# Optimization experiments

Hardware: AMD Instinct MI355X
Metric: run time of the kernel (lower is better)

Reference implementation:

```python
import jax, jax.numpy as jnp
import numpy as np

N = 50000      # nodes
E = 800000     # edges (before self-loops)
DIN = 384
D = 128        # hidden_dim == output_dim
H = 4          # heads
FH = D // H    # per-head dim
B = 64         # graphs in batch
NEG = 0.2      # LeakyReLU slope in GATConv
EPS = 1e-5     # LayerNorm eps


def setup_inputs() -> dict:
    key = jax.random.key(0)
    ks = jax.random.split(key, 24)
    s = 0.02
    inp = {
        'node_features': jax.random.normal(ks[0], (N, DIN), jnp.float32),
        'edge_index': jax.random.randint(ks[1], (2, E), 0, N, dtype=jnp.int64),
        'edge_weight': jax.random.uniform(ks[2], (E,), jnp.float32),
        'batch': jnp.sort(jax.random.randint(ks[3], (N,), 0, B, dtype=jnp.int64)),
        # input projection
        'Wp': jax.random.normal(ks[4], (DIN, D), jnp.float32) * s,
        'bp': jnp.zeros((D,), jnp.float32),
    }
    for l in range(2):
        o = 5 + l * 9
        inp[f'W{l}'] = jax.random.normal(ks[o], (D, D), jnp.float32) * s      # lin_src (shared src/dst)
        inp[f'as{l}'] = jax.random.normal(ks[o + 1], (H, FH), jnp.float32) * s  # att_src
        inp[f'ad{l}'] = jax.random.normal(ks[o + 2], (H, FH), jnp.float32) * s  # att_dst
        inp[f'We{l}'] = jax.random.normal(ks[o + 3], (D,), jnp.float32) * s   # lin_edge (edge_dim=1)
        inp[f'ae{l}'] = jax.random.normal(ks[o + 4], (H, FH), jnp.float32) * s  # att_edge
        inp[f'b{l}'] = jnp.zeros((D,), jnp.float32)                           # GATConv bias
        inp[f'g{l}'] = jnp.ones((D,), jnp.float32)                            # LayerNorm gamma
        inp[f'be{l}'] = jnp.zeros((D,), jnp.float32)                          # LayerNorm beta
    return inp


def _gat(x, src, dst, ew, W, a_s, a_d, We, a_e, b):
    """PyG GATConv(in, D/H, heads=H, edge_dim=1), eval mode. ew includes self-loops."""
    n = x.shape[0]
    h = (x @ W).reshape(n, H, FH)                      # [N,H,FH]
    a_src = jnp.einsum('nhf,hf->nh', h, a_s)           # [N,H]
    a_dst = jnp.einsum('nhf,hf->nh', h, a_d)
    e = (ew[:, None] * We[None, :]).reshape(-1, H, FH)  # edge_dim=1 linear, no bias
    a_eg = jnp.einsum('ehf,hf->eh', e, a_e)            # [E,H]
    alpha = jax.nn.leaky_relu(a_src[src] + a_dst[dst] + a_eg, NEG)
    # softmax over incoming edges of each dst node
    amax = jax.ops.segment_max(alpha, dst, num_segments=n)
    amax = jnp.where(jnp.isfinite(amax), amax, 0.0)
    ex = jnp.exp(alpha - amax[dst])
    denom = jax.ops.segment_sum(ex, dst, num_segments=n)
    coef = ex / (denom[dst] + 1e-16)                   # [E,H]
    msg = h[src] * coef[..., None]                     # [E,H,FH]
    out = jax.ops.segment_sum(msg, dst, num_segments=n).reshape(n, D)
    return out + b


def _ln(x, g, b):
    mu = x.mean(-1, keepdims=True)
    v = ((x - mu) ** 2).mean(-1, keepdims=True)
    return (x - mu) * jax.lax.rsqrt(v + EPS) * g + b


def reference(node_features, edge_index, edge_weight, batch, Wp, bp,
              W0, as0, ad0, We0, ae0, b0, g0, be0,
              W1, as1, ad1, We1, ae1, b1, g1, be1):
    n = node_features.shape[0]
    # PyG GATConv add_self_loops=True, fill_value='mean' for edge_attr
    loop = jnp.arange(n, dtype=edge_index.dtype)
    src = jnp.concatenate([edge_index[0], loop])
    dst = jnp.concatenate([edge_index[1], loop])
    ew = jnp.concatenate([edge_weight, jnp.full((n,), edge_weight.mean(), edge_weight.dtype)])

    x = node_features @ Wp + bp
    for (W, a_s, a_d, We, a_e, b, g, be) in (
        (W0, as0, ad0, We0, ae0, b0, g0, be0),
        (W1, as1, ad1, We1, ae1, b1, g1, be1),
    ):
        res = x
        y = _gat(x, src, dst, ew, W, a_s, a_d, We, a_e, b)
        y = jax.nn.elu(_ln(y, g, be))
        x = y + res  # shapes match (hidden == output)

    # global_mean_pool
    s = jax.ops.segment_sum(x, batch, num_segments=B)
    c = jax.ops.segment_sum(jnp.ones((n,), x.dtype), batch, num_segments=B)
    return s / jnp.maximum(c, 1.0)[:, None]
```

## Files before the change

kernel.cpp:

```cpp
#include <hip/hip_runtime.h>

#define N_NODES 50000
#define N_EDGES 800000
#define DIN 384
#define DH 128
#define NB 64
#define NEG 0.2f

__device__ __forceinline__ float bf2f(unsigned short u) {
    return __uint_as_float((unsigned)u << 16);
}
__device__ __forceinline__ unsigned short f2bf(float x) {
    unsigned u = __float_as_uint(x);
    return (unsigned short)((u + 0x7fff + ((u >> 16) & 1)) >> 16);
}
__device__ __forceinline__ float sel4(float4 v, int k) {
    float r = v.x;
    r = (k == 1) ? v.y : r;
    r = (k == 2) ? v.z : r;
    r = (k == 3) ? v.w : r;
    return r;
}
using us8 = __attribute__((ext_vector_type(8))) unsigned short;
using short8 = __attribute__((ext_vector_type(8))) short;
using f32x4  = __attribute__((ext_vector_type(4))) float;

__global__ __launch_bounds__(256) void histew_kernel(const int* __restrict__ dst,
        const float* __restrict__ ew, int* __restrict__ cnt,
        int* __restrict__ rank, float* __restrict__ ews,
        const float* __restrict__ Wp, const float* __restrict__ W0,
        const float* __restrict__ W1,
        const float* __restrict__ as0, const float* __restrict__ ad0,
        const float* __restrict__ as1, const float* __restrict__ ad1,
        unsigned short* __restrict__ Wtp, unsigned short* __restrict__ Wt0,
        unsigned short* __restrict__ Wt1) {
    __shared__ float sred[4];
    const int tid = threadIdx.x;
    const int pi = blockIdx.x * 256 + tid;
    if (blockIdx.x < 192) {
        const int k = pi >> 7, n = pi & 127;
        Wtp[(size_t)n * DIN + k] = f2bf(Wp[pi]);
        if (pi < DH * DH) {
            Wt0[(size_t)n * DH + k] = f2bf(W0[pi]);
            Wt1[(size_t)n * DH + k] = f2bf(W1[pi]);
        }
    } else if (blockIdx.x < 196) {
        const int b = blockIdx.x - 192;
        const int layer = b >> 1, sd = b & 1;
        const float* Ws = layer ? W1 : W0;
        const float* av = layer ? (sd ? ad1 : as1) : (sd ? ad0 : as0);
        unsigned short* Wt = layer ? Wt1 : Wt0;
        #pragma unroll
        for (int rep = 0; rep < 2; ++rep) {
            const int idx = rep * 256 + tid;
            const int k = idx >> 2, hd = idx & 3;
            float s = 0.f;
            for (int f = 0; f < 32; ++f)
                s += Ws[k * DH + hd * 32 + f] * av[hd * 32 + f];
            Wt[(size_t)(128 + sd * 4 + hd) * DH + k] = f2bf(s);
        }
    }
    float v = 0.0f;
    for (int i = blockIdx.x * 256 + tid; i < N_EDGES; i += gridDim.x * 256) {
        rank[i] = atomicAdd(&cnt[dst[i]], 1);
        v += ew[i];
    }
    #pragma unroll
    for (int o = 32; o; o >>= 1) v += __shfl_down(v, o, 64);
    if ((tid & 63) == 0) sred[tid >> 6] = v;
    __syncthreads();
    if (tid == 0) atomicAdd(ews, sred[0] + sred[1] + sred[2] + sred[3]);
}

#define SB 196
__global__ __launch_bounds__(256) void scan_a(const int* __restrict__ cnt,
                       int* __restrict__ scanned, int* __restrict__ bsums,
                       const float* __restrict__ We0, const float* __restrict__ ae0,
                       const float* __restrict__ We1, const float* __restrict__ ae1,
                       const float* __restrict__ ews, float* __restrict__ consts) {
    __shared__ int s[256];
    const int tid = threadIdx.x;
    if (blockIdx.x < SB) {
        int i = blockIdx.x * 256 + tid;
        int v = (i < N_NODES) ? cnt[i] : 0;
        s[tid] = v; __syncthreads();
        for (int o = 1; o < 256; o <<= 1) {
            int t = (tid >= o) ? s[tid - o] : 0;
            __syncthreads();
            s[tid] += t;
            __syncthreads();
        }
        if (i < N_NODES) scanned[i] = s[tid] - v;
        if (tid == 255) bsums[blockIdx.x] = s[255];
    } else if (tid < 64) {
        const int l = tid;
        float p00 = We0[l] * ae0[l];
        float p01 = We0[l + 64] * ae0[l + 64];
        float p10 = We1[l] * ae1[l];
        float p11 = We1[l + 64] * ae1[l + 64];
        #pragma unroll
        for (int o = 1; o < 32; o <<= 1) {
            p00 += __shfl_xor(p00, o, 64); p01 += __shfl_xor(p01, o, 64);
            p10 += __shfl_xor(p10, o, 64); p11 += __shfl_xor(p11, o, 64);
        }
        const float c0 = __shfl(p00, 0, 64), c1 = __shfl(p00, 32, 64);
        const float c2 = __shfl(p01, 0, 64), c3 = __shfl(p01, 32, 64);
        const float d0 = __shfl(p10, 0, 64), d1 = __shfl(p10, 32, 64);
        const float d2 = __shfl(p11, 0, 64), d3 = __shfl(p11, 32, 64);
        if (l == 0) {
            consts[0] = c0; consts[1] = c1; consts[2] = c2; consts[3] = c3;
            consts[4] = d0; consts[5] = d1; consts[6] = d2; consts[7] = d3;
            consts[8] = ews[0] * (1.0f / N_EDGES);
        }
    }
}

__global__ __launch_bounds__(256) void scan_bc(const int* __restrict__ scanned,
                        const int* __restrict__ bsums,
                        const int* __restrict__ cnt, int* __restrict__ ptr) {
    __shared__ int red[4];
    const int tid = threadIdx.x;
    int part = 0;
    for (int j = tid; j < blockIdx.x; j += 256) part += bsums[j];
    #pragma unroll
    for (int o = 32; o; o >>= 1) part += __shfl_down(part, o, 64);
    if ((tid & 63) == 0) red[tid >> 6] = part;
    __syncthreads();
    const int off = red[0] + red[1] + red[2] + red[3];
    const int i = blockIdx.x * 256 + tid;
    if (i < N_NODES) {
        const int p = scanned[i] + off;
        ptr[i] = p;
        if (i == N_NODES - 1) ptr[N_NODES] = p + cnt[i];
    }
}

#define PROJB 782
__global__ __launch_bounds__(256) void fillproj_kernel(
    const int* __restrict__ src, const int* __restrict__ dst,
    const float* __restrict__ ew, const int* __restrict__ rank,
    const int* __restrict__ ptr, int2* __restrict__ recE,
    const float* __restrict__ A, const unsigned short* __restrict__ Wt,
    const float* __restrict__ bias, float* __restrict__ C,
    unsigned short* __restrict__ Cb, int M)
{
    constexpr int K = DIN, BM = 64, BK = 32, LS = 40;
    __shared__ unsigned short As[BM * LS];
    __shared__ unsigned short Bs[DH * LS];
    const int tid = threadIdx.x;

    if (blockIdx.x >= PROJB) {
        const int e0 = ((blockIdx.x - PROJB) * 256 + tid) * 4;
        if (e0 >= N_EDGES) return;
        const int4 d4 = *(const int4*)(dst + e0);
        const int4 s4 = *(const int4*)(src + e0);
        const int4 r4 = *(const int4*)(rank + e0);
        const float4 w4 = *(const float4*)(ew + e0);
        recE[ptr[d4.x] + r4.x] = make_int2(s4.x, __float_as_int(w4.x));
        recE[ptr[d4.y] + r4.y] = make_int2(s4.y, __float_as_int(w4.y));
        recE[ptr[d4.z] + r4.z] = make_int2(s4.z, __float_as_int(w4.z));
        recE[ptr[d4.w] + r4.w] = make_int2(s4.w, __float_as_int(w4.w));
        return;
    }

    const int w = tid >> 6, l = tid & 63;
    const int lane16 = l & 15, quad = l >> 4;
    const int m0 = blockIdx.x * BM;

    f32x4 acc[8] = {};

    const int ar = tid >> 2, a4 = tid & 3;
    int arow = m0 + ar; if (arow >= M) arow = M - 1;
    const float* Ap = A + (size_t)arow * K;

    for (int k0 = 0; k0 < K; k0 += BK) {
        __syncthreads();
        #pragma unroll
        for (int i = 0; i < 2; ++i) {
            const int f4 = a4 + 4 * i;
            float4 v = *(const float4*)(Ap + k0 + f4 * 4);
            ushort4 u = {f2bf(v.x), f2bf(v.y), f2bf(v.z), f2bf(v.w)};
            *(ushort4*)&As[ar * LS + f4 * 4] = u;
        }
        #pragma unroll
        for (int i = 0; i < 2; ++i) {
            const int idx = tid + 256 * i;
            const int bn = idx >> 2, seg = idx & 3;
            us8 v = *(const us8*)(Wt + (size_t)bn * K + k0 + seg * 8);
            *(us8*)&Bs[bn * LS + seg * 8] = v;
        }
        __syncthreads();
        short8 afr = *(short8*)&As[(w * 16 + lane16) * LS + quad * 8];
        #pragma unroll
        for (int nt = 0; nt < 8; ++nt) {
            short8 bf = *(short8*)&Bs[(nt * 16 + lane16) * LS + quad * 8];
            acc[nt] = __builtin_amdgcn_mfma_f32_16x16x32_bf16(afr, bf, acc[nt], 0, 0, 0);
        }
    }

    const int orow0 = m0 + w * 16 + quad * 4;
    #pragma unroll
    for (int nt = 0; nt < 8; ++nt) {
        const int col = nt * 16 + lane16;
        const float bv = bias[col];
        #pragma unroll
        for (int r = 0; r < 4; ++r) {
            const int row = orow0 + r;
            if (row < M) {
                const float v = acc[nt][r] + bv;
                C[(size_t)row * DH + col] = v;
                Cb[(size_t)row * DH + col] = f2bf(v);
            }
        }
    }
}

__global__ __launch_bounds__(256) void mfma_gemm_layer(
    const unsigned short* __restrict__ Ab, const unsigned short* __restrict__ Wt,
    unsigned short* __restrict__ Hout, int M,
    float* __restrict__ asrc_o, float* __restrict__ adst_o)
{
    constexpr int K = DH, BM = 64, BK = 32, LS = 40;
    __shared__ unsigned short As[BM * LS];
    __shared__ unsigned short Bs[144 * LS];

    const int tid = threadIdx.x;
    const int w = tid >> 6, l = tid & 63;
    const int lane16 = l & 15, quad = l >> 4;
    const int m0 = blockIdx.x * BM;

    f32x4 acc[9] = {};

    const int ar = tid >> 2, aseg = tid & 3;
    int arow = m0 + ar; if (arow >= M) arow = M - 1;
    const unsigned short* Ap = Ab + (size_t)arow * K;

    for (int k0 = 0; k0 < K; k0 += BK) {
        __syncthreads();
        {
            us8 v = *(const us8*)(Ap + k0 + aseg * 8);
            *(us8*)&As[ar * LS + aseg * 8] = v;
        }
        #pragma unroll
        for (int i = 0; i < 3; ++i) {
            const int idx = tid + 256 * i;
            if (idx < 576) {
                const int bn = idx >> 2, seg = idx & 3;
                us8 v = *(const us8*)(Wt + (size_t)bn * K + k0 + seg * 8);
                *(us8*)&Bs[bn * LS + seg * 8] = v;
            }
        }
        __syncthreads();
        short8 af = *(short8*)&As[(w * 16 + lane16) * LS + quad * 8];
        #pragma unroll
        for (int nt = 0; nt < 9; ++nt) {
            short8 bf = *(short8*)&Bs[(nt * 16 + lane16) * LS + quad * 8];
            acc[nt] = __builtin_amdgcn_mfma_f32_16x16x32_bf16(af, bf, acc[nt], 0, 0, 0);
        }
    }

    const int orow0 = m0 + w * 16 + quad * 4;
    #pragma unroll
    for (int nt = 0; nt < 8; ++nt) {
        const int col = nt * 16 + lane16;
        #pragma unroll
        for (int r = 0; r < 4; ++r) {
            const int row = orow0 + r;
            if (row < M)
                Hout[(size_t)row * DH + col] = f2bf(acc[nt][r]);
        }
    }
    #pragma unroll
    for (int r = 0; r < 4; ++r) {
        const int row = orow0 + r;
        if (row < M && lane16 < 8) {
            if (lane16 < 4) asrc_o[(size_t)row * 4 + lane16] = acc[8][r];
            else            adst_o[(size_t)row * 4 + (lane16 - 4)] = acc[8][r];
        }
    }
}

__device__ __forceinline__ void msg_node(
    const int n, const int c8, const int hd8,
    const float cc_l, const float ewm,
    const unsigned short* __restrict__ h,
    const float* __restrict__ asrc, const float* __restrict__ adst,
    const float* __restrict__ xres,
    const int* __restrict__ indptr, const int2* __restrict__ recE,
    const float* __restrict__ bias, const float* __restrict__ gamma,
    const float* __restrict__ beta, float z[8])
{
    const unsigned short* hb = h + c8 * 8;
    const int st = indptr[n];
    const int deg = indptr[n + 1] - st;
    const float ad_l = adst[(size_t)n * 4 + hd8];
    const float as_l = asrc[(size_t)n * 4 + hd8];

    float a0 = as_l + ad_l + ewm * cc_l;
    a0 = a0 > 0.f ? a0 : NEG * a0;
    const float pv0_l = __expf(a0);

    float dsum = 0.f;
    float acc8[8];
    {
        us8 u = *(const us8*)(hb + (size_t)n * DH);
        #pragma unroll
        for (int i = 0; i < 8; ++i) acc8[i] = pv0_l * bf2f(u[i]);
    }

    const int2* rq = recE + st;
    int e = 0;
    for (; e + 3 < deg; e += 4) {
        const int2 r0 = rq[e],     r1 = rq[e + 1];
        const int2 r2 = rq[e + 2], r3 = rq[e + 3];
        const float av0 = asrc[(size_t)r0.x * 4 + hd8];
        const float av1 = asrc[(size_t)r1.x * 4 + hd8];
        const float av2 = asrc[(size_t)r2.x * 4 + hd8];
        const float av3 = asrc[(size_t)r3.x * 4 + hd8];
        us8 u0 = *(const us8*)(hb + (size_t)r0.x * DH);
        us8 u1 = *(const us8*)(hb + (size_t)r1.x * DH);
        us8 u2 = *(const us8*)(hb + (size_t)r2.x * DH);
        us8 u3 = *(const us8*)(hb + (size_t)r3.x * DH);
        float al0 = av0 + ad_l + __int_as_float(r0.y) * cc_l;
        float al1 = av1 + ad_l + __int_as_float(r1.y) * cc_l;
        float al2 = av2 + ad_l + __int_as_float(r2.y) * cc_l;
        float al3 = av3 + ad_l + __int_as_float(r3.y) * cc_l;
        al0 = al0 > 0.f ? al0 : NEG * al0;
        al1 = al1 > 0.f ? al1 : NEG * al1;
        al2 = al2 > 0.f ? al2 : NEG * al2;
        al3 = al3 > 0.f ? al3 : NEG * al3;
        const float c0 = __expf(al0), c1 = __expf(al1);
        const float c2 = __expf(al2), c3 = __expf(al3);
        dsum += (c0 + c1) + (c2 + c3);
        #pragma unroll
        for (int i = 0; i < 8; ++i)
            acc8[i] = fmaf(c0, bf2f(u0[i]),
                      fmaf(c1, bf2f(u1[i]),
                      fmaf(c2, bf2f(u2[i]),
                      fmaf(c3, bf2f(u3[i]), acc8[i]))));
    }
    for (; e < deg; ++e) {
        const int2 r = rq[e];
        const float av = asrc[(size_t)r.x * 4 + hd8];
        us8 u = *(const us8*)(hb + (size_t)r.x * DH);
        float al = av + ad_l + __int_as_float(r.y) * cc_l;
        al = al > 0.f ? al : NEG * al;
        const float c = __expf(al);
        dsum += c;
        #pragma unroll
        for (int i = 0; i < 8; ++i) acc8[i] = fmaf(c, bf2f(u[i]), acc8[i]);
    }

    const float inv_d = 1.0f / (dsum + pv0_l + 1e-16f);
    const float4 b4a = *(const float4*)(bias + c8 * 8);
    const float4 b4b = *(const float4*)(bias + c8 * 8 + 4);
    float y[8];
    y[0] = acc8[0] * inv_d + b4a.x; y[1] = acc8[1] * inv_d + b4a.y;
    y[2] = acc8[2] * inv_d + b4a.z; y[3] = acc8[3] * inv_d + b4a.w;
    y[4] = acc8[4] * inv_d + b4b.x; y[5] = acc8[5] * inv_d + b4b.y;
    y[6] = acc8[6] * inv_d + b4b.z; y[7] = acc8[7] * inv_d + b4b.w;

    float s1 = 0.f, s2 = 0.f;
    #pragma unroll
    for (int i = 0; i < 8; ++i) { s1 += y[i]; s2 += y[i] * y[i]; }
    #pragma unroll
    for (int o = 1; o < 16; o <<= 1) {
        s1 += __shfl_xor(s1, o, 64);
        s2 += __shfl_xor(s2, o, 64);
    }
    const float mu = s1 * (1.0f / DH);
    const float var = s2 * (1.0f / DH) - mu * mu;
    const float rs = rsqrtf(var + 1e-5f);

    const float4 g4a = *(const float4*)(gamma + c8 * 8);
    const float4 g4b = *(const float4*)(gamma + c8 * 8 + 4);
    const float4 e4a = *(const float4*)(beta + c8 * 8);
    const float4 e4b = *(const float4*)(beta + c8 * 8 + 4);
    const float4 r4a = *(const float4*)(xres + (size_t)n * DH + c8 * 8);
    const float4 r4b = *(const float4*)(xres + (size_t)n * DH + c8 * 8 + 4);
    const float gv[8] = {g4a.x, g4a.y, g4a.z, g4a.w, g4b.x, g4b.y, g4b.z, g4b.w};
    const float ev[8] = {e4a.x, e4a.y, e4a.z, e4a.w, e4b.x, e4b.y, e4b.z, e4b.w};
    const float rv[8] = {r4a.x, r4a.y, r4a.z, r4a.w, r4b.x, r4b.y, r4b.z, r4b.w};
    #pragma unroll
    for (int i = 0; i < 8; ++i) {
        float t = (y[i] - mu) * rs * gv[i] + ev[i];
        z[i] = (t > 0.f ? t : __expf(t) - 1.0f) + rv[i];
    }
}

#define MSG_NPB 16
__global__ __launch_bounds__(256) void msg_main_kernel(
    const unsigned short* __restrict__ h, const float* __restrict__ asrc,
    const float* __restrict__ adst, const float* __restrict__ xres,
    const int* __restrict__ indptr, const int2* __restrict__ recE,
    const float* __restrict__ consts, const int layer,
    const float* __restrict__ bias, const float* __restrict__ gamma,
    const float* __restrict__ beta, float* __restrict__ xout,
    unsigned short* __restrict__ xob)
{
    const int l = threadIdx.x & 63;
    const int wv = threadIdx.x >> 6;
    const int grp = l >> 4, c8 = l & 15, hd8 = c8 >> 2;
    const int n = blockIdx.x * MSG_NPB + wv * 4 + grp;

    const float cc_l = sel4(*(const float4*)(consts + layer * 4), hd8);
    const float ewm = consts[8];

    float z[8];
    msg_node(n, c8, hd8, cc_l, ewm, h, asrc, adst, xres, indptr, recE,
             bias, gamma, beta, z);

    *(float4*)(xout + (size_t)n * DH + c8 * 8)     = *(float4*)&z[0];
    *(float4*)(xout + (size_t)n * DH + c8 * 8 + 4) = *(float4*)&z[4];
    if (xob) {
        ushort4 ub0 = {f2bf(z[0]), f2bf(z[1]), f2bf(z[2]), f2bf(z[3])};
        ushort4 ub1 = {f2bf(z[4]), f2bf(z[5]), f2bf(z[6]), f2bf(z[7])};
        *(ushort4*)(xob + (size_t)n * DH + c8 * 8)     = ub0;
        *(ushort4*)(xob + (size_t)n * DH + c8 * 8 + 4) = ub1;
    }
}

#define PNODES 64
__global__ __launch_bounds__(128) void pool_kernel(const float* __restrict__ x,
        const int* __restrict__ batch, float* __restrict__ pool, int* __restrict__ gcnt)
{
    int t = threadIdx.x;
    int n0 = blockIdx.x * PNODES;
    if (n0 >= N_NODES) return;
    int n1 = min(n0 + PNODES, N_NODES);
    float acc = 0.f; int cn = 0;
    int curb = batch[n0];
    for (int n = n0; n < n1; ++n) {
        int b = batch[n];
        if (b != curb) {
            atomicAdd(&pool[(size_t)curb * DH + t], acc);
            if (t == 0) atomicAdd(&gcnt[curb], cn);
            acc = 0.f; cn = 0; curb = b;
        }
        acc += x[(size_t)n * DH + t];
        ++cn;
    }
    atomicAdd(&pool[(size_t)curb * DH + t], acc);
    if (t == 0) atomicAdd(&gcnt[curb], cn);
}

__global__ void div_kernel(const float* __restrict__ pool, const int* __restrict__ gcnt,
                           float* __restrict__ out)
{
    int i = blockIdx.x * blockDim.x + threadIdx.x;
    if (i < NB * DH) {
        float c = (float)gcnt[i >> 7];
        out[i] = pool[i] / fmaxf(c, 1.0f);
    }
}

extern "C" void kernel_launch(void* const* d_in, const int* in_sizes, int n_in,
                              void* d_out, int out_size, void* d_ws, size_t ws_size,
                              hipStream_t stream)
{
    const float* nf    = (const float*)d_in[0];
    const int*   esrc  = (const int*)d_in[1];
    const int*   edst  = esrc + N_EDGES;
    const float* ew    = (const float*)d_in[2];
    const int*   batch = (const int*)d_in[3];
    const float* Wp    = (const float*)d_in[4];
    const float* bp    = (const float*)d_in[5];
    const float* Wl[2]  = {(const float*)d_in[6],  (const float*)d_in[14]};
    const float* asl[2] = {(const float*)d_in[7],  (const float*)d_in[15]};
    const float* adl[2] = {(const float*)d_in[8],  (const float*)d_in[16]};
    const float* Wel[2] = {(const float*)d_in[9],  (const float*)d_in[17]};
    const float* ael[2] = {(const float*)d_in[10], (const float*)d_in[18]};
    const float* bl[2]  = {(const float*)d_in[11], (const float*)d_in[19]};
    const float* gl[2]  = {(const float*)d_in[12], (const float*)d_in[20]};
    const float* bel[2] = {(const float*)d_in[13], (const float*)d_in[21]};
    float* outp = (float*)d_out;

    char* w = (char*)d_ws;
    auto alloc = [&](size_t bytes) { char* p = w; w += (bytes + 255) & ~255ull; return p; };
    float* xA     = (float*)alloc((size_t)N_NODES * DH * 4);
    float* xB     = (float*)alloc((size_t)N_NODES * DH * 4);
    unsigned short* hbuf = (unsigned short*)alloc((size_t)N_NODES * DH * 2);
    unsigned short* xb   = (unsigned short*)alloc((size_t)N_NODES * DH * 2);
    float* asrc   = (float*)alloc((size_t)N_NODES * 4 * 4);
    float* adst   = (float*)alloc((size_t)N_NODES * 4 * 4);
    float* pool   = (float*)alloc((size_t)NB * DH * 4);
    int* gcnt     = (int*)alloc(256);
    float* ews    = (float*)alloc(256);
    int* cnt      = (int*)alloc((size_t)N_NODES * 4);
    int* scanned  = (int*)alloc((size_t)N_NODES * 4);
    int* bsums    = (int*)alloc(1024);
    int* ptr      = (int*)alloc((size_t)(N_NODES + 8) * 4);
    int* rank     = (int*)alloc((size_t)N_EDGES * 4);
    int2* recE    = (int2*)alloc((size_t)N_EDGES * 8);
    float* consts = (float*)alloc(256);
    unsigned short* Wtp = (unsigned short*)alloc((size_t)DH * DIN * 2);
    unsigned short* Wt0 = (unsigned short*)alloc((size_t)144 * DH * 2);
    unsigned short* Wt1 = (unsigned short*)alloc((size_t)144 * DH * 2);
    unsigned short* Wts[2] = {Wt0, Wt1};

    hipMemsetAsync(pool, 0, (size_t)NB * DH * 4 + 256 + 256 + (size_t)N_NODES * 4, stream);

    histew_kernel<<<1024, 256, 0, stream>>>(edst, ew, cnt, rank, ews,
                                            Wp, Wl[0], Wl[1],
                                            asl[0], adl[0], asl[1], adl[1],
                                            Wtp, Wt0, Wt1);
    scan_a<<<SB + 1, 256, 0, stream>>>(cnt, scanned, bsums,
                                       Wel[0], ael[0], Wel[1], ael[1], ews, consts);
    scan_bc<<<SB, 256, 0, stream>>>(scanned, bsums, cnt, ptr);
    fillproj_kernel<<<PROJB + (N_EDGES / 4 + 255) / 256, 256, 0, stream>>>(
        esrc, edst, ew, rank, ptr, recE, nf, Wtp, bp, xA, xb, N_NODES);

    const int gb = (N_NODES + 63) / 64;
    const int mb = N_NODES / MSG_NPB;

    mfma_gemm_layer<<<gb, 256, 0, stream>>>(xb, Wts[0], hbuf, N_NODES, asrc, adst);
    msg_main_kernel<<<mb, 256, 0, stream>>>(
        hbuf, asrc, adst, xA, ptr, recE, consts, 0,
        bl[0], gl[0], bel[0], xB, xb);

    mfma_gemm_layer<<<gb, 256, 0, stream>>>(xb, Wts[1], hbuf, N_NODES, asrc, adst);
    msg_main_kernel<<<mb, 256, 0, stream>>>(
        hbuf, asrc, adst, xB, ptr, recE, consts, 1,
        bl[1], gl[1], bel[1], xA, nullptr);

    pool_kernel<<<(N_NODES + PNODES - 1) / PNODES, 128, 0, stream>>>(xA, batch, pool, gcnt);
    div_kernel<<<(NB * DH + 255) / 256, 256, 0, stream>>>(pool, gcnt, outp);
}
```

Measured before the change: 361.1 us.

## Fuse input projection with edge histogram and CSR fill with layer-0 GEMM

The input projection GEMM now runs in the same launch as the degree histogram. It reads fp32 Wp directly and converts it to bf16 in LDS, which removes the separate pre-transposed Wtp buffer and the dependency on it. The CSR edge fill moves from the projection kernel into the layer-0 transform GEMM launch. The goal is to remove one kernel launch and let independent work overlap across blocks. The trade-off is that each projection block now reloads and converts Wp with strided, uncoalesced-per-k loads.

```diff
diff --git a/kernel.cpp b/kernel.cpp
--- a/kernel.cpp
+++ b/kernel.cpp
@@ -25,51 +25,116 @@
 using short8 = __attribute__((ext_vector_type(8))) short;
 using f32x4  = __attribute__((ext_vector_type(4))) float;
 
-__global__ __launch_bounds__(256) void histew_kernel(const int* __restrict__ dst,
-        const float* __restrict__ ew, int* __restrict__ cnt,
-        int* __restrict__ rank, float* __restrict__ ews,
-        const float* __restrict__ Wp, const float* __restrict__ W0,
-        const float* __restrict__ W1,
-        const float* __restrict__ as0, const float* __restrict__ ad0,
-        const float* __restrict__ as1, const float* __restrict__ ad1,
-        unsigned short* __restrict__ Wtp, unsigned short* __restrict__ Wt0,
-        unsigned short* __restrict__ Wt1) {
-    __shared__ float sred[4];
+#define PROJB 782
+#define HISTB 1024
+__global__ __launch_bounds__(256) void histproj_kernel(
+    const int* __restrict__ dst, const float* __restrict__ ew,
+    int* __restrict__ cnt, int* __restrict__ rank, float* __restrict__ ews,
+    const float* __restrict__ W0, const float* __restrict__ W1,
+    const float* __restrict__ as0, const float* __restrict__ ad0,
+    const float* __restrict__ as1, const float* __restrict__ ad1,
+    unsigned short* __restrict__ Wt0, unsigned short* __restrict__ Wt1,
+    const float* __restrict__ A, const float* __restrict__ Wp,
+    const float* __restrict__ bias, float* __restrict__ C,
+    unsigned short* __restrict__ Cb, int M)
+{
     const int tid = threadIdx.x;
-    const int pi = blockIdx.x * 256 + tid;
-    if (blockIdx.x < 192) {
-        const int k = pi >> 7, n = pi & 127;
-        Wtp[(size_t)n * DIN + k] = f2bf(Wp[pi]);
-        if (pi < DH * DH) {
+
+    if (blockIdx.x >= PROJB) {
+        __shared__ float sred[4];
+        const int hb = blockIdx.x - PROJB;
+        if (hb < 64) {
+            const int pi = hb * 256 + tid;
+            const int k = pi >> 7, n = pi & 127;
             Wt0[(size_t)n * DH + k] = f2bf(W0[pi]);
             Wt1[(size_t)n * DH + k] = f2bf(W1[pi]);
-        }
-    } else if (blockIdx.x < 196) {
-        const int b = blockIdx.x - 192;
-        const int layer = b >> 1, sd = b & 1;
-        const float* Ws = layer ? W1 : W0;
-        const float* av = layer ? (sd ? ad1 : as1) : (sd ? ad0 : as0);
-        unsigned short* Wt = layer ? Wt1 : Wt0;
-        #pragma unroll
-        for (int rep = 0; rep < 2; ++rep) {
-            const int idx = rep * 256 + tid;
-            const int k = idx >> 2, hd = idx & 3;
-            float s = 0.f;
-            for (int f = 0; f < 32; ++f)
-                s += Ws[k * DH + hd * 32 + f] * av[hd * 32 + f];
-            Wt[(size_t)(128 + sd * 4 + hd) * DH + k] = f2bf(s);
-        }
-    }
-    float v = 0.0f;
-    for (int i = blockIdx.x * 256 + tid; i < N_EDGES; i += gridDim.x * 256) {
-        rank[i] = atomicAdd(&cnt[dst[i]], 1);
-        v += ew[i];
-    }
-    #pragma unroll
-    for (int o = 32; o; o >>= 1) v += __shfl_down(v, o, 64);
-    if ((tid & 63) == 0) sred[tid >> 6] = v;
-    __syncthreads();
-    if (tid == 0) atomicAdd(ews, sred[0] + sred[1] + sred[2] + sred[3]);
+        } else if (hb < 68) {
+            const int b = hb - 64;
+            const int layer = b >> 1, sd = b & 1;
+            const float* Ws = layer ? W1 : W0;
+            const float* av = layer ? (sd ? ad1 : as1) : (sd ? ad0 : as0);
+            unsigned short* Wt = layer ? Wt1 : Wt0;
+            #pragma unroll
+            for (int rep = 0; rep < 2; ++rep) {
+                const int idx = rep * 256 + tid;
+                const int k = idx >> 2, hd = idx & 3;
+                float s = 0.f;
+                for (int f = 0; f < 32; ++f)
+                    s += Ws[k * DH + hd * 32 + f] * av[hd * 32 + f];
+                Wt[(size_t)(128 + sd * 4 + hd) * DH + k] = f2bf(s);
+            }
+        }
+        float v = 0.0f;
+        for (int i = hb * 256 + tid; i < N_EDGES; i += HISTB * 256) {
+            rank[i] = atomicAdd(&cnt[dst[i]], 1);
+            v += ew[i];
+        }
+        #pragma unroll
+        for (int o = 32; o; o >>= 1) v += __shfl_down(v, o, 64);
+        if ((tid & 63) == 0) sred[tid >> 6] = v;
+        __syncthreads();
+        if (tid == 0) atomicAdd(ews, sred[0] + sred[1] + sred[2] + sred[3]);
+        return;
+    }
+
+    constexpr int K = DIN, BM = 64, BK = 32, LS = 40;
+    __shared__ unsigned short As[BM * LS];
+    __shared__ unsigned short Bs[DH * LS];
+
+    const int w = tid >> 6, l = tid & 63;
+    const int lane16 = l & 15, quad = l >> 4;
+    const int m0 = blockIdx.x * BM;
+
+    f32x4 acc[8] = {};
+
+    const int ar = tid >> 2, a4 = tid & 3;
+    int arow = m0 + ar; if (arow >= M) arow = M - 1;
+    const float* Ap = A + (size_t)arow * K;
+    const int bn = tid & 127, bq = tid >> 7;
+
+    for (int k0 = 0; k0 < K; k0 += BK) {
+        __syncthreads();
+        #pragma unroll
+        for (int i = 0; i < 2; ++i) {
+            const int f4 = a4 + 4 * i;
+            float4 v = *(const float4*)(Ap + k0 + f4 * 4);
+            ushort4 u = {f2bf(v.x), f2bf(v.y), f2bf(v.z), f2bf(v.w)};
+            *(ushort4*)&As[ar * LS + f4 * 4] = u;
+        }
+        #pragma unroll
+        for (int i = 0; i < 4; ++i) {
+            const int kq = bq + 2 * i;
+            float v0 = Wp[(size_t)(k0 + kq * 4 + 0) * DH + bn];
+            float v1 = Wp[(size_t)(k0 + kq * 4 + 1) * DH + bn];
+            float v2 = Wp[(size_t)(k0 + kq * 4 + 2) * DH + bn];
+            float v3 = Wp[(size_t)(k0 + kq * 4 + 3) * DH + bn];
+            ushort4 u = {f2bf(v0), f2bf(v1), f2bf(v2), f2bf(v3)};
+            *(ushort4*)&Bs[bn * LS + kq * 4] = u;
+        }
+        __syncthreads();
+        short8 afr = *(short8*)&As[(w * 16 + lane16) * LS + quad * 8];
+        #pragma unroll
+        for (int nt = 0; nt < 8; ++nt) {
+            short8 bf = *(short8*)&Bs[(nt * 16 + lane16) * LS + quad * 8];
+            acc[nt] = __builtin_amdgcn_mfma_f32_16x16x32_bf16(afr, bf, acc[nt], 0, 0, 0);
+        }
+    }
+
+    const int orow0 = m0 + w * 16 + quad * 4;
+    #pragma unroll
+    for (int nt = 0; nt < 8; ++nt) {
+        const int col = nt * 16 + lane16;
+        const float bv = bias[col];
+        #pragma unroll
+        for (int r = 0; r < 4; ++r) {
+            const int row = orow0 + r;
+            if (row < M) {
+                const float v = acc[nt][r] + bv;
+                C[(size_t)row * DH + col] = v;
+                Cb[(size_t)row * DH + col] = f2bf(v);
+            }
+        }
+    }
 }
 
 #define SB 196
@@ -135,22 +200,22 @@
     }
 }
 
-#define PROJB 782
-__global__ __launch_bounds__(256) void fillproj_kernel(
+#define GEMMB 782
+__global__ __launch_bounds__(256) void gemmfill_kernel(
+    const unsigned short* __restrict__ Ab, const unsigned short* __restrict__ Wt,
+    unsigned short* __restrict__ Hout, int M,
+    float* __restrict__ asrc_o, float* __restrict__ adst_o,
     const int* __restrict__ src, const int* __restrict__ dst,
     const float* __restrict__ ew, const int* __restrict__ rank,
-    const int* __restrict__ ptr, int2* __restrict__ recE,
-    const float* __restrict__ A, const unsigned short* __restrict__ Wt,
-    const float* __restrict__ bias, float* __restrict__ C,
-    unsigned short* __restrict__ Cb, int M)
-{
-    constexpr int K = DIN, BM = 64, BK = 32, LS = 40;
+    const int* __restrict__ ptr, int2* __restrict__ recE)
+{
+    constexpr int K = DH, BM = 64, BK = 32, LS = 40;
     __shared__ unsigned short As[BM * LS];
-    __shared__ unsigned short Bs[DH * LS];
+    __shared__ unsigned short Bs[144 * LS];
     const int tid = threadIdx.x;
 
-    if (blockIdx.x >= PROJB) {
-        const int e0 = ((blockIdx.x - PROJB) * 256 + tid) * 4;
+    if (blockIdx.x >= GEMMB) {
+        const int e0 = ((blockIdx.x - GEMMB) * 256 + tid) * 4;
         if (e0 >= N_EDGES) return;
         const int4 d4 = *(const int4*)(dst + e0);
         const int4 s4 = *(const int4*)(src + e0);
@@ -163,68 +228,6 @@
         return;
     }
 
-    const int w = tid >> 6, l = tid & 63;
-    const int lane16 = l & 15, quad = l >> 4;
-    const int m0 = blockIdx.x * BM;
-
-    f32x4 acc[8] = {};
-
-    const int ar = tid >> 2, a4 = tid & 3;
-    int arow = m0 + ar; if (arow >= M) arow = M - 1;
-    const float* Ap = A + (size_t)arow * K;
-
-    for (int k0 = 0; k0 < K; k0 += BK) {
-        __syncthreads();
-        #pragma unroll
-        for (int i = 0; i < 2; ++i) {
-            const int f4 = a4 + 4 * i;
-            float4 v = *(const float4*)(Ap + k0 + f4 * 4);
-            ushort4 u = {f2bf(v.x), f2bf(v.y), f2bf(v.z), f2bf(v.w)};
-            *(ushort4*)&As[ar * LS + f4 * 4] = u;
-        }
-        #pragma unroll
-        for (int i = 0; i < 2; ++i) {
-            const int idx = tid + 256 * i;
-            const int bn = idx >> 2, seg = idx & 3;
-            us8 v = *(const us8*)(Wt + (size_t)bn * K + k0 + seg * 8);
-            *(us8*)&Bs[bn * LS + seg * 8] = v;
-        }
-        __syncthreads();
-        short8 afr = *(short8*)&As[(w * 16 + lane16) * LS + quad * 8];
-        #pragma unroll
-        for (int nt = 0; nt < 8; ++nt) {
-            short8 bf = *(short8*)&Bs[(nt * 16 + lane16) * LS + quad * 8];
-            acc[nt] = __builtin_amdgcn_mfma_f32_16x16x32_bf16(afr, bf, acc[nt], 0, 0, 0);
-        }
-    }
-
-    const int orow0 = m0 + w * 16 + quad * 4;
-    #pragma unroll
-    for (int nt = 0; nt < 8; ++nt) {
-        const int col = nt * 16 + lane16;
-        const float bv = bias[col];
-        #pragma unroll
-        for (int r = 0; r < 4; ++r) {
-            const int row = orow0 + r;
-            if (row < M) {
-                const float v = acc[nt][r] + bv;
-                C[(size_t)row * DH + col] = v;
-                Cb[(size_t)row * DH + col] = f2bf(v);
-            }
-        }
-    }
-}
-
-__global__ __launch_bounds__(256) void mfma_gemm_layer(
-    const unsigned short* __restrict__ Ab, const unsigned short* __restrict__ Wt,
-    unsigned short* __restrict__ Hout, int M,
-    float* __restrict__ asrc_o, float* __restrict__ adst_o)
-{
-    constexpr int K = DH, BM = 64, BK = 32, LS = 40;
-    __shared__ unsigned short As[BM * LS];
-    __shared__ unsigned short Bs[144 * LS];
-
-    const int tid = threadIdx.x;
     const int w = tid >> 6, l = tid & 63;
     const int lane16 = l & 15, quad = l >> 4;
     const int m0 = blockIdx.x * BM;
@@ -493,32 +496,33 @@
     int* rank     = (int*)alloc((size_t)N_EDGES * 4);
     int2* recE    = (int2*)alloc((size_t)N_EDGES * 8);
     float* consts = (float*)alloc(256);
-    unsigned short* Wtp = (unsigned short*)alloc((size_t)DH * DIN * 2);
     unsigned short* Wt0 = (unsigned short*)alloc((size_t)144 * DH * 2);
     unsigned short* Wt1 = (unsigned short*)alloc((size_t)144 * DH * 2);
     unsigned short* Wts[2] = {Wt0, Wt1};
 
     hipMemsetAsync(pool, 0, (size_t)NB * DH * 4 + 256 + 256 + (size_t)N_NODES * 4, stream);
 
-    histew_kernel<<<1024, 256, 0, stream>>>(edst, ew, cnt, rank, ews,
-                                            Wp, Wl[0], Wl[1],
-                                            asl[0], adl[0], asl[1], adl[1],
-                                            Wtp, Wt0, Wt1);
+    histproj_kernel<<<PROJB + HISTB, 256, 0, stream>>>(
+        edst, ew, cnt, rank, ews,
+        Wl[0], Wl[1], asl[0], adl[0], asl[1], adl[1], Wt0, Wt1,
+        nf, Wp, bp, xA, xb, N_NODES);
+
     scan_a<<<SB + 1, 256, 0, stream>>>(cnt, scanned, bsums,
                                        Wel[0], ael[0], Wel[1], ael[1], ews, consts);
     scan_bc<<<SB, 256, 0, stream>>>(scanned, bsums, cnt, ptr);
-    fillproj_kernel<<<PROJB + (N_EDGES / 4 + 255) / 256, 256, 0, stream>>>(
-        esrc, edst, ew, rank, ptr, recE, nf, Wtp, bp, xA, xb, N_NODES);
-
-    const int gb = (N_NODES + 63) / 64;
+
     const int mb = N_NODES / MSG_NPB;
 
-    mfma_gemm_layer<<<gb, 256, 0, stream>>>(xb, Wts[0], hbuf, N_NODES, asrc, adst);
+    gemmfill_kernel<<<GEMMB + 782, 256, 0, stream>>>(
+        xb, Wts[0], hbuf, N_NODES, asrc, adst,
+        esrc, edst, ew, rank, ptr, recE);
     msg_main_kernel<<<mb, 256, 0, stream>>>(
         hbuf, asrc, adst, xA, ptr, recE, consts, 0,
         bl[0], gl[0], bel[0], xB, xb);
 
-    mfma_gemm_layer<<<gb, 256, 0, stream>>>(xb, Wts[1], hbuf, N_NODES, asrc, adst);
+    gemmfill_kernel<<<GEMMB, 256, 0, stream>>>(
+        xb, Wts[1], hbuf, N_NODES, asrc, adst,
+        esrc, edst, ew, rank, ptr, recE);
     msg_main_kernel<<<mb, 256, 0, stream>>>(
         hbuf, asrc, adst, xB, ptr, recE, consts, 1,
         bl[1], gl[1], bel[1], xA, nullptr);
```

New measurement: 352.6 us. 2.4% less time.
